# Kernel optimization log

Measured on AMD Instinct MI355X. Metric: run time of the kernel, lower is better.

The kernel has to match this reference:

```python
import jax, jax.numpy as jnp
import numpy as np

M, K, N = 8192, 4096, 4096

def setup_inputs() -> dict:
    key = jax.random.key(0)
    k1, k2, k3, k4 = jax.random.split(key, 4)
    x = jax.random.normal(k1, (M, K), dtype=jnp.float32)
    # pre-quantized int8 weights [K, N] and per-output-channel scales [N]
    weight_q = jax.random.randint(k2, (K, N), -128, 128, dtype=jnp.int32).astype(jnp.int8)
    weight_scale = (jax.random.uniform(k3, (N,), dtype=jnp.float32) * 0.01 + 1e-4)
    bias = jax.random.normal(k4, (N,), dtype=jnp.float32) * 0.02
    return {"x": x, "weight_q": weight_q, "weight_scale": weight_scale, "bias": bias}

def reference(x, weight_q, weight_scale, bias):
    # dynamic per-row int8 quantization of activations
    max_vals = jnp.max(jnp.abs(x), axis=-1, keepdims=True)          # [M, 1]
    a_scale = jnp.maximum(max_vals / 127.0, 1e-8)                    # [M, 1]
    x_q = jnp.clip(jnp.round(x / a_scale), -128, 127).astype(jnp.int8)
    c = jnp.matmul(x_q.astype(jnp.float32), weight_q.astype(jnp.float32))  # [M, N]
    # dequantize: per-row activation scale * per-column weight scale
    c = c * a_scale * weight_scale[None, :]
    out = c.astype(x.dtype) + bias
    return out
```

## Files before the change

### kernel.cpp

```cpp
#include <hip/hip_runtime.h>


typedef int int32x4 __attribute__((ext_vector_type(4)));

#define TILE_BM 128
#define TILE_BN 128
#define TILE_BK 64

__device__ __forceinline__ void async_copy16(const void* g, void* l) {
    __builtin_amdgcn_global_load_lds(
        (const __attribute__((address_space(1))) unsigned int*)g,
        (__attribute__((address_space(3))) unsigned int*)l,
        16, 0, 0);
}

__device__ __forceinline__ int quant1(float x, float s) {
    float q = rintf(x / s);
    q = fminf(127.0f, fmaxf(-128.0f, q));
    return (int)q;
}

__global__ __launch_bounds__(256) void quant_kernel(
    const float* __restrict__ x, signed char* __restrict__ xq,
    float* __restrict__ ascale, int K)
{
    const int row = blockIdx.x;
    const int t = threadIdx.x;
    const float4* xr4 = (const float4*)(x + (size_t)row * K);

    float4 v[4];
    float mx = 0.0f;
#pragma unroll
    for (int i = 0; i < 4; ++i) {
        v[i] = xr4[t * 4 + i];
        mx = fmaxf(mx, fmaxf(fmaxf(fabsf(v[i].x), fabsf(v[i].y)),
                             fmaxf(fabsf(v[i].z), fabsf(v[i].w))));
    }
#pragma unroll
    for (int off = 32; off > 0; off >>= 1)
        mx = fmaxf(mx, __shfl_xor(mx, off, 64));
    __shared__ float wmax[4];
    if ((t & 63) == 0) wmax[t >> 6] = mx;
    __syncthreads();
    mx = fmaxf(fmaxf(wmax[0], wmax[1]), fmaxf(wmax[2], wmax[3]));

    const float s = fmaxf(mx / 127.0f, 1e-8f);
    if (t == 0) ascale[row] = s;

    int out[4];
#pragma unroll
    for (int i = 0; i < 4; ++i) {
        const int b0 = quant1(v[i].x, s);
        const int b1 = quant1(v[i].y, s);
        const int b2 = quant1(v[i].z, s);
        const int b3 = quant1(v[i].w, s);
        out[i] = (b0 & 255) | ((b1 & 255) << 8) | ((b2 & 255) << 16) | ((b3 & 255) << 24);
    }
    *(int32x4*)(xq + (size_t)row * K + t * 16) = *(const int32x4*)out;
}

__global__ __launch_bounds__(256) void transpose_pack_kernel(
    const int* __restrict__ Bq, signed char* __restrict__ Bt, int K, int N)
{
    __shared__ int lds[64 * 17];
    const int t = threadIdx.x;
    const int n0 = blockIdx.x * 64;
    const int k0 = blockIdx.y * 64;

    const int r = t >> 4;
    const int ncol = (t & 15) * 4;

    const int* src = Bq + (size_t)(k0 + 4 * r) * N + n0 + ncol;
    const int4 u0 = *(const int4*)(src);
    const int4 u1 = *(const int4*)(src + N);
    const int4 u2 = *(const int4*)(src + 2 * (size_t)N);
    const int4 u3 = *(const int4*)(src + 3 * (size_t)N);

    lds[(ncol + 0) * 17 + r] = (u0.x & 255) | ((u1.x & 255) << 8) | ((u2.x & 255) << 16) | ((u3.x & 255) << 24);
    lds[(ncol + 1) * 17 + r] = (u0.y & 255) | ((u1.y & 255) << 8) | ((u2.y & 255) << 16) | ((u3.y & 255) << 24);
    lds[(ncol + 2) * 17 + r] = (u0.z & 255) | ((u1.z & 255) << 8) | ((u2.z & 255) << 16) | ((u3.z & 255) << 24);
    lds[(ncol + 3) * 17 + r] = (u0.w & 255) | ((u1.w & 255) << 8) | ((u2.w & 255) << 16) | ((u3.w & 255) << 24);
    __syncthreads();

    const int nl = t >> 2, ch = t & 3;
    int o[4];
#pragma unroll
    for (int i = 0; i < 4; ++i) o[i] = lds[nl * 17 + ch * 4 + i];
    *(int32x4*)(Bt + (size_t)(n0 + nl) * K + k0 + ch * 16) = *(const int32x4*)o;
}

__global__ __launch_bounds__(256, 2) void gemm_i8_kernel(
    const signed char* __restrict__ Aq, const signed char* __restrict__ Bt,
    const float* __restrict__ ascale, const float* __restrict__ wscale,
    const float* __restrict__ bias, float* __restrict__ C,
    int M, int N, int K)
{
    __shared__ __align__(16) signed char As[TILE_BM * TILE_BK];
    __shared__ __align__(16) signed char Bs[TILE_BN * TILE_BK];

    const int t = threadIdx.x;
    const int lane = t & 63;
    const int w = t >> 6;
    const int wr = w >> 1, wc = w & 1;

    const int m0 = blockIdx.y * TILE_BM;
    const int n0 = blockIdx.x * TILE_BN;

    const int srow = t >> 2;
    const int schunk = (t & 3) * 16;
    const signed char* gA0 = Aq + (size_t)(m0 + srow) * K + schunk;
    const signed char* gA1 = gA0 + (size_t)64 * K;
    const signed char* gB0 = Bt + (size_t)(n0 + srow) * K + schunk;
    const signed char* gB1 = gB0 + (size_t)64 * K;
    signed char* lA0 = As + t * 16;
    signed char* lA1 = lA0 + 4096;
    signed char* lB0 = Bs + t * 16;
    signed char* lB1 = lB0 + 4096;

    const int kb16 = (lane >> 4) * 16;
    const int ml = lane & 15;
    const signed char* fA = As + (wr * 64 + ml) * TILE_BK + kb16;
    const signed char* fB = Bs + (wc * 64 + ml) * TILE_BK + kb16;

    int32x4 acc[4][4] = {};

    for (int k0 = 0; k0 < K; k0 += TILE_BK) {
        async_copy16(gA0 + k0, lA0);
        async_copy16(gA1 + k0, lA1);
        async_copy16(gB0 + k0, lB0);
        async_copy16(gB1 + k0, lB1);
        __syncthreads();

        int32x4 af[4], bf[4];
#pragma unroll
        for (int i = 0; i < 4; ++i) {
            af[i] = *(const int32x4*)(fA + i * 16 * TILE_BK);
            bf[i] = *(const int32x4*)(fB + i * 16 * TILE_BK);
        }
#pragma unroll
        for (int i = 0; i < 4; ++i)
#pragma unroll
            for (int j = 0; j < 4; ++j)
                acc[i][j] = __builtin_amdgcn_mfma_i32_16x16x64_i8(af[i], bf[j], acc[i][j], 0, 0, 0);
        __syncthreads();
    }

    const int colb = n0 + wc * 64 + ml;
    const int rowb = m0 + wr * 64 + (lane >> 4) * 4;
#pragma unroll
    for (int j = 0; j < 4; ++j) {
        const int col = colb + j * 16;
        const float ws = wscale[col];
        const float bs = bias[col];
#pragma unroll
        for (int i = 0; i < 4; ++i) {
            const int row = rowb + i * 16;
            float* cp = C + (size_t)row * N + col;
#pragma unroll
            for (int r = 0; r < 4; ++r) {
                cp[(size_t)r * N] = ((float)acc[i][j][r] * ascale[row + r]) * ws + bs;
            }
        }
    }
}

extern "C" void kernel_launch(void* const* d_in, const int* in_sizes, int n_in,
                              void* d_out, int out_size, void* d_ws, size_t ws_size,
                              hipStream_t stream) {
    const float* x      = (const float*)d_in[0];
    const int*   wq     = (const int*)d_in[1];
    const float* wscale = (const float*)d_in[2];
    const float* bias   = (const float*)d_in[3];
    float* out          = (float*)d_out;

    const int N = in_sizes[2];
    const int K = in_sizes[1] / N;
    const int M = in_sizes[0] / K;

    char* ws = (char*)d_ws;
    signed char* xq = (signed char*)ws;
    signed char* bt = (signed char*)(ws + (size_t)M * K);
    float* ascale   = (float*)(ws + (size_t)M * K + (size_t)N * K);

    quant_kernel<<<M, 256, 0, stream>>>(x, xq, ascale, K);
    transpose_pack_kernel<<<dim3(N / 64, K / 64), 256, 0, stream>>>(wq, bt, K, N);
    gemm_i8_kernel<<<dim3(N / TILE_BN, M / TILE_BM), 256, 0, stream>>>(
        xq, bt, ascale, wscale, bias, out, M, N, K);
}
```

Before: 429.0 us.

## Rewrite int8 GEMM with 256x256 tiles, double-buffered LDS pipeline and swizzle

Grows the GEMM tile to 256x256x128 with 512 threads and double-buffers LDS across 128 KiB. Global-to-LDS copies are interleaved with MFMA quarter-steps using explicit barriers, vmcnt waits and setprio. LDS is XOR-swizzled to avoid bank conflicts, and workgroup IDs are remapped across 8 groups for cache locality. The quantization kernel also switches to coalesced per-lane 4-byte stores. The risks are heavy register pressure from 32 accumulators, only 32x16 = 512 workgroups to fill the device, and ordering bugs in the hand-scheduled pipeline.

```diff
diff --git a/kernel.cpp b/kernel.cpp
--- a/kernel.cpp
+++ b/kernel.cpp
@@ -3,9 +3,9 @@
 
 typedef int int32x4 __attribute__((ext_vector_type(4)));
 
-#define TILE_BM 128
-#define TILE_BN 128
-#define TILE_BK 64
+#define TILE_BM 256
+#define TILE_BN 256
+#define TILE_BK 128
 
 __device__ __forceinline__ void async_copy16(const void* g, void* l) {
     __builtin_amdgcn_global_load_lds(
@@ -32,7 +32,7 @@
     float mx = 0.0f;
 #pragma unroll
     for (int i = 0; i < 4; ++i) {
-        v[i] = xr4[t * 4 + i];
+        v[i] = xr4[i * 256 + t];
         mx = fmaxf(mx, fmaxf(fmaxf(fabsf(v[i].x), fabsf(v[i].y)),
                              fmaxf(fabsf(v[i].z), fabsf(v[i].w))));
     }
@@ -47,16 +47,15 @@
     const float s = fmaxf(mx / 127.0f, 1e-8f);
     if (t == 0) ascale[row] = s;
 
-    int out[4];
+    int* xqr = (int*)(xq + (size_t)row * K);
 #pragma unroll
     for (int i = 0; i < 4; ++i) {
         const int b0 = quant1(v[i].x, s);
         const int b1 = quant1(v[i].y, s);
         const int b2 = quant1(v[i].z, s);
         const int b3 = quant1(v[i].w, s);
-        out[i] = (b0 & 255) | ((b1 & 255) << 8) | ((b2 & 255) << 16) | ((b3 & 255) << 24);
-    }
-    *(int32x4*)(xq + (size_t)row * K + t * 16) = *(const int32x4*)out;
+        xqr[i * 256 + t] = (b0 & 255) | ((b1 & 255) << 8) | ((b2 & 255) << 16) | ((b3 & 255) << 24);
+    }
 }
 
 __global__ __launch_bounds__(256) void transpose_pack_kernel(
@@ -89,76 +88,163 @@
     *(int32x4*)(Bt + (size_t)(n0 + nl) * K + k0 + ch * 16) = *(const int32x4*)o;
 }
 
-__global__ __launch_bounds__(256, 2) void gemm_i8_kernel(
+
+#define SBAR() do { asm volatile("" ::: "memory"); __builtin_amdgcn_s_barrier(); asm volatile("" ::: "memory"); } while (0)
+#define LGKM0() asm volatile("s_waitcnt lgkmcnt(0)" ::: "memory")
+#define VMCNT(n) asm volatile("s_waitcnt vmcnt(" #n ")" ::: "memory")
+
+#define MFMA_Q(AF, MB, NB)                                                              \
+    do {                                                                                \
+        __builtin_amdgcn_s_setprio(1);                                                  \
+        _Pragma("unroll") for (int mm = 0; mm < 4; ++mm) {                              \
+            _Pragma("unroll") for (int nn = 0; nn < 2; ++nn) {                          \
+                int32x4 v = acc[(MB) + mm][(NB) + nn];                                  \
+                v = __builtin_amdgcn_mfma_i32_16x16x64_i8(AF[mm][0], b[(NB) + nn][0], v, 0, 0, 0); \
+                v = __builtin_amdgcn_mfma_i32_16x16x64_i8(AF[mm][1], b[(NB) + nn][1], v, 0, 0, 0); \
+                acc[(MB) + mm][(NB) + nn] = v;                                          \
+            }                                                                           \
+        }                                                                               \
+        __builtin_amdgcn_s_setprio(0);                                                  \
+    } while (0)
+
+__global__ __launch_bounds__(512, 2) void gemm_i8_kernel(
     const signed char* __restrict__ Aq, const signed char* __restrict__ Bt,
     const float* __restrict__ ascale, const float* __restrict__ wscale,
     const float* __restrict__ bias, float* __restrict__ C,
     int M, int N, int K)
 {
-    __shared__ __align__(16) signed char As[TILE_BM * TILE_BK];
-    __shared__ __align__(16) signed char Bs[TILE_BN * TILE_BK];
+    __shared__ __align__(16) signed char smem[131072];
 
     const int t = threadIdx.x;
     const int lane = t & 63;
     const int w = t >> 6;
-    const int wr = w >> 1, wc = w & 1;
-
-    const int m0 = blockIdx.y * TILE_BM;
-    const int n0 = blockIdx.x * TILE_BN;
-
-    const int srow = t >> 2;
-    const int schunk = (t & 3) * 16;
-    const signed char* gA0 = Aq + (size_t)(m0 + srow) * K + schunk;
-    const signed char* gA1 = gA0 + (size_t)64 * K;
-    const signed char* gB0 = Bt + (size_t)(n0 + srow) * K + schunk;
-    const signed char* gB1 = gB0 + (size_t)64 * K;
-    signed char* lA0 = As + t * 16;
-    signed char* lA1 = lA0 + 4096;
-    signed char* lB0 = Bs + t * 16;
-    signed char* lB1 = lB0 + 4096;
-
-    const int kb16 = (lane >> 4) * 16;
-    const int ml = lane & 15;
-    const signed char* fA = As + (wr * 64 + ml) * TILE_BK + kb16;
-    const signed char* fB = Bs + (wc * 64 + ml) * TILE_BK + kb16;
-
-    int32x4 acc[4][4] = {};
-
-    for (int k0 = 0; k0 < K; k0 += TILE_BK) {
-        async_copy16(gA0 + k0, lA0);
-        async_copy16(gA1 + k0, lA1);
-        async_copy16(gB0 + k0, lB0);
-        async_copy16(gB1 + k0, lB1);
-        __syncthreads();
-
-        int32x4 af[4], bf[4];
-#pragma unroll
-        for (int i = 0; i < 4; ++i) {
-            af[i] = *(const int32x4*)(fA + i * 16 * TILE_BK);
-            bf[i] = *(const int32x4*)(fB + i * 16 * TILE_BK);
+    const int wr = w >> 2;
+    const int wc = w & 3;
+    const int ml = lane & 15, kq = lane >> 4;
+    const int lr = lane >> 3, l8 = lane & 7;
+
+    const int nbx = gridDim.x;
+    int bid = blockIdx.y * nbx + blockIdx.x;
+    const int nwg = nbx * gridDim.y;
+    if ((nwg & 7) == 0) bid = (bid & 7) * (nwg >> 3) + (bid >> 3);
+    const int m0 = (bid / nbx) * TILE_BM;
+    const int n0 = (bid % nbx) * TILE_BN;
+
+    const int srow = w * 8 + lr;
+    const int stoff = srow * 128 + l8 * 16;
+    const signed char* gA = Aq + (size_t)(m0 + srow) * K + ((l8 ^ lr) << 4);
+    const signed char* gB = Bt + (size_t)(n0 + srow) * K + ((l8 ^ lr) << 4);
+
+    auto stage = [&](int slot, int op, int h, int tk) {
+        signed char* l = smem + slot * 65536 + op * 32768 + h * 16384 + stoff;
+        const signed char* g = (op ? gB : gA) + (size_t)(h * 128) * K + (size_t)tk * TILE_BK;
+        async_copy16(g, l);
+        async_copy16(g + (size_t)64 * K, l + 8192);
+    };
+
+    const int axor = (ml & 7) << 4;
+    const int c0 = (kq * 16) ^ axor;
+    const int c1 = (64 + kq * 16) ^ axor;
+    const int aBase = (wr * 128 + ml) * 128;
+    const int bBase = 32768 + (wc * 64 + ml) * 128;
+
+    int32x4 acc[8][4] = {};
+    int32x4 a0[4][2], a1[4][2], b[4][2];
+
+    auto rdA = [&](int32x4 (&dst)[4][2], int slotoff, int mb) {
+#pragma unroll
+        for (int mm = 0; mm < 4; ++mm) {
+            const signed char* p = smem + slotoff + aBase + (mb + mm) * 2048;
+            dst[mm][0] = *(const int32x4*)(p + c0);
+            dst[mm][1] = *(const int32x4*)(p + c1);
         }
-#pragma unroll
-        for (int i = 0; i < 4; ++i)
-#pragma unroll
-            for (int j = 0; j < 4; ++j)
-                acc[i][j] = __builtin_amdgcn_mfma_i32_16x16x64_i8(af[i], bf[j], acc[i][j], 0, 0, 0);
-        __syncthreads();
+    };
+    auto rdB = [&](int slotoff) {
+#pragma unroll
+        for (int nn = 0; nn < 4; ++nn) {
+            const signed char* p = smem + slotoff + bBase + nn * 2048;
+            b[nn][0] = *(const int32x4*)(p + c0);
+            b[nn][1] = *(const int32x4*)(p + c1);
+        }
+    };
+
+    const int NI = K / (2 * TILE_BK);
+
+    stage(0, 0, 0, 0); stage(0, 0, 1, 0); stage(0, 1, 0, 0); stage(0, 1, 1, 0);
+    stage(1, 0, 0, 1); stage(1, 0, 1, 1);
+    VMCNT(4);
+    SBAR();
+
+    for (int i = 0; i < NI; ++i) {
+        const bool last = (i == NI - 1);
+        const int t1 = 2 * i + 1, t2 = 2 * i + 2, t3 = 2 * i + 3;
+
+        rdA(a0, 0, 0);
+        rdB(0);
+        stage(1, 1, 0, t1);
+        SBAR();
+        MFMA_Q(a0, 0, 0);
+        LGKM0();
+        SBAR();
+
+        rdA(a1, 0, 4);
+        stage(1, 1, 1, t1);
+        SBAR();
+        MFMA_Q(a0, 0, 2);
+        LGKM0();
+        SBAR();
+
+        if (!last) stage(0, 0, 0, t2);
+        SBAR();
+        MFMA_Q(a1, 4, 0);
+        SBAR();
+
+        if (!last) { stage(0, 0, 1, t2); VMCNT(4); }
+        else       { VMCNT(0); }
+        SBAR();
+        MFMA_Q(a1, 4, 2);
+        SBAR();
+
+        rdA(a0, 65536, 0);
+        rdB(65536);
+        if (!last) stage(0, 1, 0, t2);
+        SBAR();
+        MFMA_Q(a0, 0, 0);
+        LGKM0();
+        SBAR();
+
+        rdA(a1, 65536, 4);
+        if (!last) stage(0, 1, 1, t2);
+        SBAR();
+        MFMA_Q(a0, 0, 2);
+        LGKM0();
+        SBAR();
+
+        if (!last) stage(1, 0, 0, t3);
+        SBAR();
+        MFMA_Q(a1, 4, 0);
+        SBAR();
+
+        if (!last) { stage(1, 0, 1, t3); VMCNT(4); }
+        SBAR();
+        MFMA_Q(a1, 4, 2);
+        SBAR();
     }
 
     const int colb = n0 + wc * 64 + ml;
-    const int rowb = m0 + wr * 64 + (lane >> 4) * 4;
-#pragma unroll
-    for (int j = 0; j < 4; ++j) {
-        const int col = colb + j * 16;
-        const float ws = wscale[col];
-        const float bs = bias[col];
-#pragma unroll
-        for (int i = 0; i < 4; ++i) {
-            const int row = rowb + i * 16;
+    const int rowb = m0 + wr * 128 + kq * 4;
+#pragma unroll
+    for (int n = 0; n < 4; ++n) {
+        const int col = colb + n * 16;
+        const float wsn = wscale[col];
+        const float bsn = bias[col];
+#pragma unroll
+        for (int m = 0; m < 8; ++m) {
+            const int row = rowb + m * 16;
             float* cp = C + (size_t)row * N + col;
 #pragma unroll
             for (int r = 0; r < 4; ++r) {
-                cp[(size_t)r * N] = ((float)acc[i][j][r] * ascale[row + r]) * ws + bs;
+                cp[(size_t)r * N] = ((float)acc[m][n][r] * ascale[row + r]) * wsn + bsn;
             }
         }
     }
@@ -184,6 +270,6 @@
 
     quant_kernel<<<M, 256, 0, stream>>>(x, xq, ascale, K);
     transpose_pack_kernel<<<dim3(N / 64, K / 64), 256, 0, stream>>>(wq, bt, K, N);
-    gemm_i8_kernel<<<dim3(N / TILE_BN, M / TILE_BM), 256, 0, stream>>>(
+    gemm_i8_kernel<<<dim3(N / TILE_BN, M / TILE_BM), 512, 0, stream>>>(
         xq, bt, ascale, wscale, bias, out, M, N, K);
 }
```

Result: faster. 395.2 us (-7.9%).
